# Optimization experiments

Measured on AMD Instinct MI355X. Metric: run time of the kernel, lower is better.

The kernel has to match this reference:

```python
import jax, jax.numpy as jnp
import numpy as np

B, N, D = 4, 2048, 1024


def setup_inputs() -> dict:
    key = jax.random.key(0)
    ks = jax.random.split(key, 9)
    x = jax.random.normal(ks[0], (B, N, D), dtype=jnp.float32)
    # causal mask: True = masked (set to -inf), per dot_product_attention semantics
    mask = jnp.triu(jnp.ones((N, N), dtype=bool), k=1)
    mask = jnp.broadcast_to(mask, (B, N, N))
    scale = 1.0 / np.sqrt(D)
    Wq = jax.random.normal(ks[1], (D, D), dtype=jnp.float32) * scale
    Wk = jax.random.normal(ks[2], (D, D), dtype=jnp.float32) * scale
    Wv = jax.random.normal(ks[3], (D, D), dtype=jnp.float32) * scale
    Wo = jax.random.normal(ks[4], (D, D), dtype=jnp.float32) * scale
    bq = jnp.zeros((D,), dtype=jnp.float32)
    bk = jnp.zeros((D,), dtype=jnp.float32)
    bv = jnp.zeros((D,), dtype=jnp.float32)
    bo = jnp.zeros((D,), dtype=jnp.float32)
    return {"x": x, "mask": mask, "Wq": Wq, "bq": bq, "Wk": Wk, "bk": bk,
            "Wv": Wv, "bv": bv, "Wo": Wo, "bo": bo}


def reference(x, mask, Wq, bq, Wk, bk, Wv, bv, Wo, bo):
    # QKV projections (single-head despite docstring; module never splits heads)
    Q = x @ Wq + bq  # [b, n, d]
    K = x @ Wk + bk
    V = x @ Wv + bv
    d = K.shape[-1]
    scores = jnp.einsum('bqd,bkd->bqk', Q, K) / jnp.sqrt(jnp.asarray(d, Q.dtype))
    min_infty = jnp.finfo(scores.dtype).min
    scores = jnp.where(mask, min_infty, scores)
    weights = jax.nn.softmax(scores, axis=-1)
    attention = jnp.einsum('bqk,bkd->bqd', weights, V)
    out = attention @ Wo + bo
    return out
```

## Files before the change

### kernel.cpp

```cpp
#include <hip/hip_runtime.h>
#include <hip/hip_bf16.h>

typedef __attribute__((ext_vector_type(8))) short short8;
typedef __attribute__((ext_vector_type(4))) float f32x4;

__device__ inline float b2f(unsigned short u) {
    union { unsigned int i; float f; } c; c.i = ((unsigned int)u) << 16; return c.f;
}
__device__ inline unsigned short f2b(float f) {
    __hip_bfloat16 h = __float2bfloat16(f);
    return *reinterpret_cast<unsigned short*>(&h);
}

__device__ inline void gl_lds16(const unsigned short* g, unsigned short* ldsbase) {
    __builtin_amdgcn_global_load_lds(
        (const __attribute__((address_space(1))) unsigned int*)(g),
        (__attribute__((address_space(3))) unsigned int*)(ldsbase),
        16, 0, 0);
}

__global__ __launch_bounds__(256) void cvt_f32_bf16(
    const float* __restrict__ src, unsigned short* __restrict__ dst, int n4)
{
    int i = blockIdx.x * 256 + threadIdx.x;
    if (i >= n4) return;
    float4 v = ((const float4*)src)[i];
    union { unsigned short u[4]; unsigned long long ll; } p;
    p.u[0] = f2b(v.x); p.u[1] = f2b(v.y); p.u[2] = f2b(v.z); p.u[3] = f2b(v.w);
    ((unsigned long long*)dst)[i] = p.ll;
}

__global__ __launch_bounds__(256) void cvt_weights4(
    const float* __restrict__ s0, const float* __restrict__ s1, const float* __restrict__ s2,
    const float* __restrict__ s3,
    unsigned short* __restrict__ d0, unsigned short* __restrict__ d1,
    unsigned short* __restrict__ d2, unsigned short* __restrict__ d3)
{
    const int z = blockIdx.z;
    if (z == 3) {
        const int i = (blockIdx.y * 32 + blockIdx.x) * 256 + threadIdx.x;
        float4 v = ((const float4*)s3)[i];
        union { unsigned short u[4]; unsigned long long ll; } p;
        p.u[0] = f2b(v.x); p.u[1] = f2b(v.y); p.u[2] = f2b(v.z); p.u[3] = f2b(v.w);
        ((unsigned long long*)d3)[i] = p.ll;
        return;
    }
    const float* src = z == 0 ? s0 : z == 1 ? s1 : s2;
    unsigned short* dst = z == 0 ? d0 : z == 1 ? d1 : d2;
    __shared__ float tile[32][33];
    const int c0 = blockIdx.x * 32, r0 = blockIdx.y * 32;
    const int tx = threadIdx.x & 31, ty = threadIdx.x >> 5;
    #pragma unroll
    for (int i = ty; i < 32; i += 8)
        tile[i][tx] = src[(long)(r0 + i) * 1024 + c0 + tx];
    __syncthreads();
    #pragma unroll
    for (int i = ty; i < 32; i += 8)
        dst[(long)(c0 + i) * 1024 + r0 + tx] = f2b(tile[tx][i]);
}

__global__ __launch_bounds__(64) void make_bvo(
    const unsigned short* __restrict__ Wot, const float* __restrict__ bv,
    const float* __restrict__ bo, float* __restrict__ bvo)
{
    const int n = blockIdx.x;
    const int lane = threadIdx.x;
    const unsigned short* row = Wot + (long)n * 1024;
    float acc = 0.f;
    #pragma unroll
    for (int pass = 0; pass < 2; pass++) {
        const int k = pass * 512 + lane * 8;
        short8 wv = *(const short8*)(row + k);
        #pragma unroll
        for (int j = 0; j < 8; j++)
            acc += bv[k + j] * b2f((unsigned short)wv[j]);
    }
    #pragma unroll
    for (int off = 32; off > 0; off >>= 1) acc += __shfl_xor(acc, off, 64);
    if (lane == 0) bvo[n] = acc + bo[n];
}

#define TILE_DECLS \
    __shared__ __attribute__((aligned(16))) unsigned short As[2 * 128 * 32]; \
    __shared__ __attribute__((aligned(16))) unsigned short Bs[2 * 128 * 32]; \
    const int t = threadIdx.x, lane = t & 63, w = t >> 6; \
    const int wr = w >> 1, wc = w & 1; \
    const int lrow = lane & 15, quad = lane >> 4; \
    f32x4 acc[4][4]; \
    _Pragma("unroll") for (int i = 0; i < 4; i++) \
        _Pragma("unroll") for (int j = 0; j < 4; j++) \
            acc[i][j] = (f32x4){0.f, 0.f, 0.f, 0.f};

#define TILE_KLOOP(gA, lda, gB, ldb, Keff) \
    for (int k0 = 0; k0 < (Keff); k0 += 64) { \
        _Pragma("unroll") for (int p = 0; p < 2; p++) \
            _Pragma("unroll") for (int h = 0; h < 2; h++) { \
                gl_lds16((gA) + (long)h * 16 * (lda) + k0 + p * 32, \
                         &As[p * 4096 + (w * 32 + h * 16) * 32]); \
                gl_lds16((gB) + (long)h * 16 * (ldb) + k0 + p * 32, \
                         &Bs[p * 4096 + (w * 32 + h * 16) * 32]); \
            } \
        __syncthreads(); \
        _Pragma("unroll") for (int p = 0; p < 2; p++) { \
            short8 af[4], bfr[4]; \
            _Pragma("unroll") for (int mi = 0; mi < 4; mi++) \
                af[mi] = *(const short8*)&As[p * 4096 + (wr * 64 + mi * 16 + lrow) * 32 + quad * 8]; \
            _Pragma("unroll") for (int ni = 0; ni < 4; ni++) \
                bfr[ni] = *(const short8*)&Bs[p * 4096 + (wc * 64 + ni * 16 + lrow) * 32 + quad * 8]; \
            _Pragma("unroll") for (int mi = 0; mi < 4; mi++) \
                _Pragma("unroll") for (int ni = 0; ni < 4; ni++) \
                    acc[mi][ni] = __builtin_amdgcn_mfma_f32_16x16x32_bf16( \
                        af[mi], bfr[ni], acc[mi][ni], 0, 0, 0); \
        } \
        __syncthreads(); \
    }

__global__ __launch_bounds__(256) void qkv_proj(
    const unsigned short* __restrict__ A,
    const unsigned short* __restrict__ Wqt, const unsigned short* __restrict__ Wkt,
    const unsigned short* __restrict__ Wvot,
    const float* __restrict__ bq, const float* __restrict__ bk,
    unsigned short* __restrict__ Q, unsigned short* __restrict__ Km,
    unsigned short* __restrict__ Vot)
{
    const int bm = blockIdx.x, bn = blockIdx.y;
    const int r = bn >> 3, bnn = bn & 7;
    const unsigned short* Bt = (r == 0) ? Wqt : (r == 1) ? Wkt : Wvot;
    const float* bias = (r == 0) ? bq : (r == 1) ? bk : nullptr;
    const int m0 = bm * 128, n0 = bnn * 128;

    TILE_DECLS

    const unsigned short* gA = A  + (long)(m0 + w * 32 + (lane >> 2)) * 1024 + (lane & 3) * 8;
    const unsigned short* gB = Bt + (long)(n0 + w * 32 + (lane >> 2)) * 1024 + (lane & 3) * 8;
    TILE_KLOOP(gA, 1024, gB, 1024, 1024)

    #pragma unroll
    for (int mi = 0; mi < 4; mi++) {
        const int m = m0 + wr * 64 + mi * 16 + quad * 4;
        #pragma unroll
        for (int ni = 0; ni < 4; ni++) {
            const int n = n0 + wc * 64 + ni * 16 + lrow;
            const float bvl = bias ? bias[n] : 0.f;
            if (r < 2) {
                unsigned short* out = (r == 0) ? Q : Km;
                #pragma unroll
                for (int rg = 0; rg < 4; rg++)
                    out[(long)(m + rg) * 1024 + n] = f2b(acc[mi][ni][rg] + bvl);
            } else {
                #pragma unroll
                for (int rg = 0; rg < 4; rg++)
                    Vot[(long)n * 8192 + m + rg] = f2b(acc[mi][ni][rg]);
            }
        }
    }
}

template<bool TRI, bool KCAUSAL, int OMODE>
__global__ __launch_bounds__(256) void gemm128(
    const unsigned short* __restrict__ A, const unsigned short* __restrict__ Bt,
    const float* __restrict__ bias, void* __restrict__ Cv,
    int K, int lda, int ldb, int ldc, long sA, long sB, long sC, float scale)
{
    int bm, bn, bz;
    if (TRI) {
        const int q = blockIdx.x;
        bm = (int)((sqrtf(8.f * q + 1.f) - 1.f) * 0.5f);
        while ((bm + 1) * (bm + 2) / 2 <= q) bm++;
        while (bm * (bm + 1) / 2 > q) bm--;
        bn = q - bm * (bm + 1) / 2;
        bz = blockIdx.y;
    } else {
        bm = KCAUSAL ? (gridDim.x - 1 - blockIdx.x) : blockIdx.x;
        bn = blockIdx.y; bz = blockIdx.z;
    }
    A  += (long)bz * sA;
    Bt += (long)bz * sB;
    const int m0 = bm * 128, n0 = bn * 128;

    TILE_DECLS

    const int Keff = KCAUSAL ? ((bm + 1) * 128 < K ? (bm + 1) * 128 : K) : K;
    const unsigned short* gA = A  + (long)(m0 + w * 32 + (lane >> 2)) * lda + (lane & 3) * 8;
    const unsigned short* gB = Bt + (long)(n0 + w * 32 + (lane >> 2)) * ldb + (lane & 3) * 8;
    TILE_KLOOP(gA, lda, gB, ldb, Keff)

    #pragma unroll
    for (int mi = 0; mi < 4; mi++) {
        const int m = m0 + wr * 64 + mi * 16 + quad * 4;
        #pragma unroll
        for (int ni = 0; ni < 4; ni++) {
            const int n = n0 + wc * 64 + ni * 16 + lrow;
            const float bvl = bias ? bias[n] : 0.f;
            #pragma unroll
            for (int rg = 0; rg < 4; rg++) {
                const float val = acc[mi][ni][rg] * scale + bvl;
                if (OMODE == 1)
                    ((float*)Cv)[(long)bz * sC + (long)(m + rg) * ldc + n] = val;
                else
                    ((unsigned short*)Cv)[(long)bz * sC + (long)(m + rg) * ldc + n] = f2b(val);
            }
        }
    }
}

__global__ __launch_bounds__(256) void softmax_causal(unsigned short* __restrict__ S)
{
    const long row = blockIdx.x;
    const int i = (int)(row & 2047);
    unsigned short* base = S + row * 2048;
    const int t = threadIdx.x;
    const int padded = ((i >> 7) + 1) << 7;
    const int j0 = t * 8;
    const bool active = j0 < padded;

    __shared__ float red[4];

    float v[8];
    if (active) {
        short8 s8 = *(const short8*)(base + j0);
        #pragma unroll
        for (int jj = 0; jj < 8; jj++)
            v[jj] = (j0 + jj <= i) ? b2f((unsigned short)s8[jj]) : -3.0e38f;
    } else {
        #pragma unroll
        for (int jj = 0; jj < 8; jj++) v[jj] = -3.0e38f;
    }

    float lmax = v[0];
    #pragma unroll
    for (int jj = 1; jj < 8; jj++) lmax = fmaxf(lmax, v[jj]);
    #pragma unroll
    for (int off = 32; off > 0; off >>= 1) lmax = fmaxf(lmax, __shfl_xor(lmax, off, 64));
    if ((t & 63) == 0) red[t >> 6] = lmax;
    __syncthreads();
    const float gmax = fmaxf(fmaxf(red[0], red[1]), fmaxf(red[2], red[3]));
    __syncthreads();

    float lsum = 0.f;
    #pragma unroll
    for (int jj = 0; jj < 8; jj++) {
        v[jj] = (v[jj] > -1.0e37f) ? __expf(v[jj] - gmax) : 0.f;
        lsum += v[jj];
    }
    #pragma unroll
    for (int off = 32; off > 0; off >>= 1) lsum += __shfl_xor(lsum, off, 64);
    if ((t & 63) == 0) red[t >> 6] = lsum;
    __syncthreads();
    const float inv = 1.0f / (red[0] + red[1] + red[2] + red[3]);

    if (active) {
        short8 p8;
        #pragma unroll
        for (int jj = 0; jj < 8; jj++) p8[jj] = (short)f2b(v[jj] * inv);
        *(short8*)(base + j0) = p8;
    }
}

extern "C" void kernel_launch(void* const* d_in, const int* in_sizes, int n_in,
                              void* d_out, int out_size, void* d_ws, size_t ws_size,
                              hipStream_t stream)
{
    const float* x  = (const float*)d_in[0];
    const float* Wq = (const float*)d_in[2];
    const float* bq = (const float*)d_in[3];
    const float* Wk = (const float*)d_in[4];
    const float* bk = (const float*)d_in[5];
    const float* Wv = (const float*)d_in[6];
    const float* bv = (const float*)d_in[7];
    const float* Wo = (const float*)d_in[8];
    const float* bo = (const float*)d_in[9];

    unsigned short* ws = (unsigned short*)d_ws;
    const long XSZ = 8192L * 1024;
    const long WSZ = 1024L * 1024;
    unsigned short* xb   = ws;
    unsigned short* Wqt  = ws + XSZ;
    unsigned short* Wkt  = Wqt + WSZ;
    unsigned short* Wot  = Wkt + WSZ;
    unsigned short* Wvb  = Wot + WSZ;
    unsigned short* Wvot = Wvb + WSZ;
    unsigned short* Q    = Wvot + WSZ;
    unsigned short* Km   = Q + XSZ;
    unsigned short* Vot  = Km + XSZ;
    unsigned short* S    = Vot + XSZ;
    float*          bvo  = (float*)(S + 4L * 2048 * 2048);

    const dim3 blk(256);

    cvt_f32_bf16<<<dim3(8192), blk, 0, stream>>>(x, xb, (int)(XSZ / 4));
    cvt_weights4<<<dim3(32, 32, 4), blk, 0, stream>>>(
        Wq, Wk, Wo, Wv, Wqt, Wkt, Wot, Wvb);
    make_bvo    <<<dim3(1024), dim3(64), 0, stream>>>(Wot, bv, bo, bvo);

    gemm128<false, false, 0><<<dim3(8, 8, 1), blk, 0, stream>>>(
        Wot, Wvb, nullptr, Wvot, 1024, 1024, 1024, 1024, 0, 0, 0, 1.f);

    qkv_proj<<<dim3(64, 24), blk, 0, stream>>>(
        xb, Wqt, Wkt, Wvot, bq, bk, Q, Km, Vot);

    gemm128<true, false, 0><<<dim3(136, 4), blk, 0, stream>>>(
        Q, Km, nullptr, S, 1024, 1024, 1024, 2048,
        2048L * 1024, 2048L * 1024, 2048L * 2048, 0.03125f);

    softmax_causal<<<dim3(4 * 2048), blk, 0, stream>>>(S);

    gemm128<false, true, 1><<<dim3(16, 8, 4), blk, 0, stream>>>(
        S, Vot, bvo, (float*)d_out, 2048, 2048, 8192, 1024,
        2048L * 2048, 2048, 2048L * 1024, 1.f);
}
```

Baseline: 342.3 us.

## Replace 128x128 GEMM tiles with 64x128 tiles and grid-based causal skipping

Replaces the 128x128 gemm128 kernel with a gemm64 kernel that uses 64x128 output tiles, its own double-slab LDS k-loop (64 k per iteration), and 2x4 MFMA accumulators per wave. The triangular blockIdx decode for the QK^T scores is replaced by a full 2D grid where blocks above the causal diagonal return early. The goal is more blocks for better CU occupancy and finer causal granularity in the PV GEMM. In exchange there is less data reuse per tile, more total global loads, and wasted launches of blocks that exit immediately.

```diff
diff --git a/kernel.cpp b/kernel.cpp
--- a/kernel.cpp
+++ b/kernel.cpp
@@ -156,38 +156,69 @@
     }
 }
 
-template<bool TRI, bool KCAUSAL, int OMODE>
-__global__ __launch_bounds__(256) void gemm128(
+template<bool CAUSAL2, bool KCAUSAL, int OMODE>
+__global__ __launch_bounds__(256) void gemm64(
     const unsigned short* __restrict__ A, const unsigned short* __restrict__ Bt,
     const float* __restrict__ bias, void* __restrict__ Cv,
     int K, int lda, int ldb, int ldc, long sA, long sB, long sC, float scale)
 {
-    int bm, bn, bz;
-    if (TRI) {
-        const int q = blockIdx.x;
-        bm = (int)((sqrtf(8.f * q + 1.f) - 1.f) * 0.5f);
-        while ((bm + 1) * (bm + 2) / 2 <= q) bm++;
-        while (bm * (bm + 1) / 2 > q) bm--;
-        bn = q - bm * (bm + 1) / 2;
-        bz = blockIdx.y;
-    } else {
-        bm = KCAUSAL ? (gridDim.x - 1 - blockIdx.x) : blockIdx.x;
-        bn = blockIdx.y; bz = blockIdx.z;
-    }
+    const int bm = KCAUSAL ? (gridDim.x - 1 - blockIdx.x) : blockIdx.x;
+    const int bn = blockIdx.y, bz = blockIdx.z;
+    if (CAUSAL2 && bm < 2 * bn) return;
     A  += (long)bz * sA;
     Bt += (long)bz * sB;
-    const int m0 = bm * 128, n0 = bn * 128;
-
-    TILE_DECLS
-
-    const int Keff = KCAUSAL ? ((bm + 1) * 128 < K ? (bm + 1) * 128 : K) : K;
-    const unsigned short* gA = A  + (long)(m0 + w * 32 + (lane >> 2)) * lda + (lane & 3) * 8;
+    const int m0 = bm * 64, n0 = bn * 128;
+
+    __shared__ __attribute__((aligned(16))) unsigned short As[2 * 64 * 32];
+    __shared__ __attribute__((aligned(16))) unsigned short Bs[2 * 128 * 32];
+
+    const int t = threadIdx.x, lane = t & 63, w = t >> 6;
+    const int wr = w >> 1, wc = w & 1;
+    const int lrow = lane & 15, quad = lane >> 4;
+
+    f32x4 acc[2][4];
+    #pragma unroll
+    for (int i = 0; i < 2; i++)
+        #pragma unroll
+        for (int j = 0; j < 4; j++)
+            acc[i][j] = (f32x4){0.f, 0.f, 0.f, 0.f};
+
+    const int KeffRaw = KCAUSAL ? ((bm >> 1) + 1) * 128 : K;
+    const int Keff = KeffRaw < K ? KeffRaw : K;
+
+    const unsigned short* gA = A  + (long)(m0 + w * 16 + (lane >> 2)) * lda + (lane & 3) * 8;
     const unsigned short* gB = Bt + (long)(n0 + w * 32 + (lane >> 2)) * ldb + (lane & 3) * 8;
-    TILE_KLOOP(gA, lda, gB, ldb, Keff)
-
-    #pragma unroll
-    for (int mi = 0; mi < 4; mi++) {
-        const int m = m0 + wr * 64 + mi * 16 + quad * 4;
+
+    for (int k0 = 0; k0 < Keff; k0 += 64) {
+        #pragma unroll
+        for (int p = 0; p < 2; p++) {
+            gl_lds16(gA + k0 + p * 32, &As[p * 2048 + (w * 16) * 32]);
+            gl_lds16(gB + k0 + p * 32, &Bs[p * 4096 + (w * 32) * 32]);
+            gl_lds16(gB + (long)16 * ldb + k0 + p * 32, &Bs[p * 4096 + (w * 32 + 16) * 32]);
+        }
+        __syncthreads();
+        #pragma unroll
+        for (int p = 0; p < 2; p++) {
+            short8 af[2], bfr[4];
+            #pragma unroll
+            for (int mi = 0; mi < 2; mi++)
+                af[mi] = *(const short8*)&As[p * 2048 + (wr * 32 + mi * 16 + lrow) * 32 + quad * 8];
+            #pragma unroll
+            for (int ni = 0; ni < 4; ni++)
+                bfr[ni] = *(const short8*)&Bs[p * 4096 + (wc * 64 + ni * 16 + lrow) * 32 + quad * 8];
+            #pragma unroll
+            for (int mi = 0; mi < 2; mi++)
+                #pragma unroll
+                for (int ni = 0; ni < 4; ni++)
+                    acc[mi][ni] = __builtin_amdgcn_mfma_f32_16x16x32_bf16(
+                        af[mi], bfr[ni], acc[mi][ni], 0, 0, 0);
+        }
+        __syncthreads();
+    }
+
+    #pragma unroll
+    for (int mi = 0; mi < 2; mi++) {
+        const int m = m0 + wr * 32 + mi * 16 + quad * 4;
         #pragma unroll
         for (int ni = 0; ni < 4; ni++) {
             const int n = n0 + wc * 64 + ni * 16 + lrow;
@@ -293,19 +324,19 @@
         Wq, Wk, Wo, Wv, Wqt, Wkt, Wot, Wvb);
     make_bvo    <<<dim3(1024), dim3(64), 0, stream>>>(Wot, bv, bo, bvo);
 
-    gemm128<false, false, 0><<<dim3(8, 8, 1), blk, 0, stream>>>(
+    gemm64<false, false, 0><<<dim3(16, 8, 1), blk, 0, stream>>>(
         Wot, Wvb, nullptr, Wvot, 1024, 1024, 1024, 1024, 0, 0, 0, 1.f);
 
     qkv_proj<<<dim3(64, 24), blk, 0, stream>>>(
         xb, Wqt, Wkt, Wvot, bq, bk, Q, Km, Vot);
 
-    gemm128<true, false, 0><<<dim3(136, 4), blk, 0, stream>>>(
+    gemm64<true, false, 0><<<dim3(32, 16, 4), blk, 0, stream>>>(
         Q, Km, nullptr, S, 1024, 1024, 1024, 2048,
         2048L * 1024, 2048L * 1024, 2048L * 2048, 0.03125f);
 
     softmax_causal<<<dim3(4 * 2048), blk, 0, stream>>>(S);
 
-    gemm128<false, true, 1><<<dim3(16, 8, 4), blk, 0, stream>>>(
+    gemm64<false, true, 1><<<dim3(32, 8, 4), blk, 0, stream>>>(
         S, Vot, bvo, (float*)d_out, 2048, 2048, 8192, 1024,
         2048L * 2048, 2048, 2048L * 1024, 1.f);
 }
```

Result: no change. 347.6 us (+1.5%).
